# Optimization experiments

Measured on AMD Instinct MI355X. Metric: run time of the kernel, lower is better.

The kernel has to match this reference:

```python
import jax, jax.numpy as jnp
import numpy as np
import math

DIM = 1024      # dim == dim_attn (required by value-reshape)
HEAD = 16
KV = 128        # K_v routing slots
HD = DIM // HEAD
N = 50000       # number of nodes


def setup_inputs() -> dict:
    key = jax.random.key(0)
    ks = jax.random.split(key, 8)
    s = lambda fan_in: 1.0 / np.sqrt(fan_in)
    return {
        "x": jax.random.normal(ks[0], (N, DIM), jnp.float32),
        "node_index": jax.random.normal(ks[1], (N, 4), jnp.float32),
        # nn.Linear(dim, dim_attn)
        "Wq": jax.random.normal(ks[2], (DIM, DIM), jnp.float32) * s(DIM),
        "bq": jnp.zeros((DIM,), jnp.float32),
        # nn.Parameter key (K_v, head, head_dim), torch.randn init
        "key_p": jax.random.normal(ks[3], (KV, HEAD, HD), jnp.float32),
        # nn.Linear(dim, dim)
        "Wv": jax.random.normal(ks[4], (DIM, DIM), jnp.float32) * s(DIM),
        "bv": jnp.zeros((DIM,), jnp.float32),
        # gate params, shape (head, 1)
        "alpha": jnp.full((HEAD, 1), math.log(9.0), jnp.float32),
        "beta": jnp.full((HEAD, 1), math.log(0.01), jnp.float32),
        # nn.Linear(4, head*K_v)
        "Wb": jax.random.normal(ks[5], (HEAD * KV, 4), jnp.float32) * s(4),
        "bb": jnp.zeros((HEAD * KV,), jnp.float32),
    }


def _mh_sinkhorn(A, num_iters=3, eps=0.05):
    # A: (N, H, K). Faithful to the per-head torch sinkhorn (Q transposed to
    # (K, N)): row sums are over the node axis, col sums over the slot axis.
    n = A.shape[0]
    k = A.shape[2]
    Q = jnp.exp(A / eps)
    Q = Q / jnp.sum(Q, axis=(0, 2), keepdims=True)          # total-sum norm per head
    for _ in range(num_iters):
        Q = Q / jnp.sum(Q, axis=0, keepdims=True) / k       # rows of Q.T (per slot)
        Q = Q / jnp.sum(Q, axis=2, keepdims=True) / n       # cols of Q.T (per node)
    return Q * n


def reference(x, node_index, Wq, bq, key_p, Wv, bv, alpha, beta, Wb, bb):
    n = x.shape[0]
    q = (x @ Wq.T + bq).reshape(n, HEAD, HD)
    attn = jnp.einsum('nhd,rhd->nhr', q, key_p) / np.float32(np.sqrt(HD))
    bias = (node_index @ Wb.T + bb).reshape(n, HEAD, KV)
    attn = attn + bias                                       # (n, H, K_v)
    xv = (x @ Wv.T + bv).reshape(n, HEAD, HD)
    v = jnp.einsum('nhr,nhd->rhd', jax.nn.sigmoid(attn), xv)  # (K_v, H, D)
    cons = _mh_sinkhorn(jax.nn.softmax(attn, axis=-1))
    v = jnp.einsum('nhr,rhd->nhd', cons, v)
    out = jax.nn.sigmoid(alpha) * xv + jax.nn.sigmoid(beta) * v  # (H,1) broadcasts
    return out.reshape(n, DIM)
```

## Files before the change

### kernel.cpp

```cpp
#include <hip/hip_runtime.h>

#define N_NODES 50000
#define MPAD    50176
#define DIM     1024
#define HEAD    16
#define KV      128
#define HD      64
#define NGRP    98

typedef unsigned short ushort_t;
typedef short short8 __attribute__((ext_vector_type(8)));
typedef float f32x4 __attribute__((ext_vector_type(4)));

__device__ inline unsigned short f2bf(float f){
  union { float f; unsigned u; } v; v.f = f;
  unsigned u = v.u;
  unsigned r = (u + 0x7FFFu + ((u >> 16) & 1u)) >> 16;
  return (unsigned short)r;
}
__device__ inline float bf2f(unsigned u16){
  union { unsigned u; float f; } v; v.u = (u16 & 0xFFFFu) << 16; return v.f;
}

__device__ inline void gload_lds16(const void* g, void* l){
  __builtin_amdgcn_global_load_lds(
      (const __attribute__((address_space(1))) void*)g,
      (__attribute__((address_space(3))) void*)l, 16, 0, 0);
}

__device__ inline short8 frag64(const ushort_t* lds, int row, int kk, int lane){
  int c  = kk*4 + (lane >> 4);
  int cc = c ^ (row & 7);
  return *(const short8*)(lds + row*64 + cc*8);
}
__device__ inline short8 frag128(const ushort_t* lds, int row, int kk, int lane){
  int c  = kk*4 + (lane >> 4);
  int cc = c ^ (row & 7);
  return *(const short8*)(lds + row*128 + cc*8);
}

__global__ void k_zero(float* p, int n){
  int i = blockIdx.x*256 + threadIdx.x;
  if (i < n) p[i] = 0.f;
}

__global__ void k_prep_x(const float* __restrict__ x, ushort_t* __restrict__ x_bf){
  int idx = blockIdx.x*256 + threadIdx.x;
  int row = idx >> 7, c = idx & 127;
  const float4* s = (const float4*)(x + (size_t)row*1024 + c*8);
  float4 f0 = s[0], f1 = s[1];
  short8 v;
  v[0]=(short)f2bf(f0.x); v[1]=(short)f2bf(f0.y); v[2]=(short)f2bf(f0.z); v[3]=(short)f2bf(f0.w);
  v[4]=(short)f2bf(f1.x); v[5]=(short)f2bf(f1.y); v[6]=(short)f2bf(f1.z); v[7]=(short)f2bf(f1.w);
  int sc = (c & ~7) | ((c ^ row) & 7);
  *(short8*)(x_bf + (size_t)row*1024 + sc*8) = v;
}

__global__ void k_prep_w(const float* __restrict__ Wq, const float* __restrict__ Wv,
                         ushort_t* __restrict__ w_bf){
  int idx = blockIdx.x*256 + threadIdx.x;
  int j = idx >> 10, k = idx & 1023;
  float v = (j < 1024) ? Wq[idx] : Wv[(size_t)(j-1024)*1024 + k];
  int d = k & 63;
  int scol = (k & ~63) | ((((d>>3) ^ (j & 7)) & 7) << 3) | (d & 7);
  w_bf[(size_t)j*1024 + scol] = f2bf(v);
}

__global__ void k_prep_key(const float* __restrict__ key_p, ushort_t* __restrict__ key_bf){
  int idx = blockIdx.x*256 + threadIdx.x;
  int h = idx >> 13, rem = idx & 8191;
  int r = rem >> 6, d = rem & 63;
  float v = key_p[(size_t)(r*HEAD + h)*HD + d];
  int pos = ((((d>>3) ^ (r & 7)) & 7) << 3) | (d & 7);
  key_bf[(size_t)h*8192 + r*64 + pos] = f2bf(v);
}

__global__ void k_vreduce(const float* __restrict__ vp, float* __restrict__ vout){
  int i = blockIdx.x*256 + threadIdx.x;
  float s = 0.f;
  for (int gg = 0; gg < NGRP; ++gg) s += vp[(size_t)gg*131072 + i];
  vout[i] = s;
}

template<int HALF>
__global__ __launch_bounds__(512) void k_gemm(const ushort_t* __restrict__ x_bf,
    const ushort_t* __restrict__ w_bf, const float* __restrict__ bq,
    const float* __restrict__ bv, ushort_t* __restrict__ q_bf, float* xv_out){
  extern __shared__ char gsm[];
  ushort_t* As = (ushort_t*)gsm;
  ushort_t* Bs = (ushort_t*)(gsm + 65536);
  const int tid = threadIdx.x, lane = tid & 63;
  const int wid = tid >> 6, wr = wid >> 2, wc = wid & 3;
  int b = blockIdx.x;
  int wg = (b & 7)*98 + (b >> 3);
  const int bm0 = (wg >> 2) * 256;
  const int bn0 = HALF*1024 + (wg & 3) * 256;

  f32x4 acc[8][4];
  #pragma unroll
  for (int m=0;m<8;m++)
    #pragma unroll
    for (int n=0;n<4;n++) acc[m][n] = (f32x4){0.f,0.f,0.f,0.f};

  const ushort_t* asrc = x_bf + (size_t)bm0*1024;
  const ushort_t* bsrc = w_bf + (size_t)bn0*1024;

#define STAGE(kt, bi)                                                    \
  { _Pragma("unroll")                                                    \
    for (int it=0; it<4; ++it){                                          \
      int chunk = it*512 + tid;                                          \
      int r = chunk >> 3, c = chunk & 7;                                 \
      gload_lds16(asrc + (size_t)r*1024 + (kt)*64 + c*8,                 \
                  As + (bi)*16384 + chunk*8);                            \
    }                                                                    \
    _Pragma("unroll")                                                    \
    for (int it=0; it<4; ++it){                                          \
      int chunk = it*512 + tid;                                          \
      int r = chunk >> 3, c = chunk & 7;                                 \
      gload_lds16(bsrc + (size_t)r*1024 + (kt)*64 + c*8,                 \
                  Bs + (bi)*16384 + chunk*8);                            \
    }                                                                    \
  }

  STAGE(0, 0);
  STAGE(1, 1);

  for (int kt = 0; kt < 16; ++kt){
    const int cur = kt & 1;
    if (kt == 15) { asm volatile("s_waitcnt vmcnt(0)" ::: "memory"); }
    else          { asm volatile("s_waitcnt vmcnt(8)" ::: "memory"); }
    __builtin_amdgcn_s_barrier();

    const ushort_t* ab  = As + cur*16384;
    const ushort_t* bb_ = Bs + cur*16384;
    #pragma unroll
    for (int kk=0;kk<2;kk++){
      short8 bfr[4];
      #pragma unroll
      for (int n=0;n<4;n++) bfr[n] = frag64(bb_, wc*64 + n*16 + (lane&15), kk, lane);
      #pragma unroll
      for (int m=0;m<8;m++){
        short8 af = frag64(ab, wr*128 + m*16 + (lane&15), kk, lane);
        #pragma unroll
        for (int n=0;n<4;n++)
          acc[m][n] = __builtin_amdgcn_mfma_f32_16x16x32_bf16(af, bfr[n], acc[m][n], 0,0,0);
      }
    }
    __builtin_amdgcn_s_barrier();
    if (kt + 2 < 16) STAGE(kt+2, cur);
  }
#undef STAGE

  __syncthreads();

  float biasv[4];
  #pragma unroll
  for (int n=0;n<4;n++){
    int col = bn0 + wc*64 + n*16 + (lane & 15);
    biasv[n] = (HALF == 0) ? bq[col] : bv[col - 1024];
  }

  if (HALF == 0){
    ushort_t* img = (ushort_t*)gsm;
    #pragma unroll
    for (int n=0;n<4;n++){
      int lcol = wc*64 + n*16 + (lane & 15);
      int d = lcol & 63;
      #pragma unroll
      for (int m=0;m<8;m++){
        #pragma unroll
        for (int j=0;j<4;j++){
          int lrow = wr*128 + m*16 + (lane>>4)*4 + j;
          int sc = (lcol & ~63) | ((((d>>3) ^ (lrow & 7)) & 7) << 3) | (d & 7);
          img[lrow*256 + sc] = f2bf(acc[m][n][j] + biasv[n]);
        }
      }
    }
    __syncthreads();
    #pragma unroll
    for (int it=0; it<16; ++it){
      int r  = it*16 + (tid >> 5);
      int ch = tid & 31;
      short8 v = *(const short8*)(img + r*256 + ch*8);
      *(short8*)(q_bf + (size_t)(bm0 + r)*1024 + bn0 + ch*8) = v;
    }
  } else {
    #pragma unroll
    for (int n=0;n<4;n++){
      int col = bn0 + wc*64 + n*16 + (lane & 15);
      #pragma unroll
      for (int m=0;m<8;m++){
        #pragma unroll
        for (int j=0;j<4;j++){
          int row = bm0 + wr*128 + m*16 + (lane>>4)*4 + j;
          if (row < N_NODES)
            xv_out[(size_t)row*1024 + (col - 1024)] = acc[m][n][j] + biasv[n];
        }
      }
    }
  }
}

__global__ __launch_bounds__(256) void k_s1(const ushort_t* __restrict__ q_bf,
    const ushort_t* __restrict__ key_bf, const float* __restrict__ ni,
    const float* __restrict__ Wb, const float* __restrict__ bb,
    const float* __restrict__ cs_in, float* __restrict__ cs_out){
  __shared__ ushort_t key_lds[128*64];
  __shared__ float col_acc[4][128];
  const int tid = threadIdx.x, lane = tid & 63, wid = tid >> 6;
  const int h   = blockIdx.x & 15;
  const int blk = blockIdx.x >> 4;
  const int gw  = blk*4 + wid;
  const int cl  = lane & 15, rg = lane >> 4;

  #pragma unroll
  for (int it = 0; it < 4; ++it){
    int chunk = it*256 + tid;
    gload_lds16(key_bf + (size_t)h*8192 + chunk*8, key_lds + chunk*8);
  }

  float wbv[8][4], bbr[8], wv[8];
  #pragma unroll
  for (int n=0;n<8;n++){
    int r = h*128 + n*16 + cl;
    float4 w4 = *(const float4*)(Wb + (size_t)r*4);
    wbv[n][0]=w4.x; wbv[n][1]=w4.y; wbv[n][2]=w4.z; wbv[n][3]=w4.w;
    bbr[n] = bb[r];
    wv[n]  = 1.f/(128.f*cs_in[r]);
  }
  float cs_acc[8];
  #pragma unroll
  for (int n=0;n<8;n++) cs_acc[n] = 0.f;

  __syncthreads();

  const int g0 = gw*4;
  short8 qc[2], qn[2];
  { int row = g0*16 + cl;
    #pragma unroll
    for (int kk=0;kk<2;kk++){
      int c = (kk*4+rg) ^ (row & 7);
      qc[kk] = *(const short8*)(q_bf + (size_t)row*1024 + h*64 + c*8);
    } }

  for (int u = 0; u < 4; ++u){
    const int i0 = (g0+u)*16;
    if (u+1 < 4){
      int row = i0 + 16 + cl;
      #pragma unroll
      for (int kk=0;kk<2;kk++){
        int c = (kk*4+rg) ^ (row & 7);
        qn[kk] = *(const short8*)(q_bf + (size_t)row*1024 + h*64 + c*8);
      }
    }
    float4 ni4[4];
    #pragma unroll
    for (int j=0;j<4;j++){
      int row = i0 + rg*4 + j;
      if (row < N_NODES) ni4[j] = *(const float4*)(ni + (size_t)row*4);
      else { ni4[j].x=0.f; ni4[j].y=0.f; ni4[j].z=0.f; ni4[j].w=0.f; }
    }
    f32x4 acc[8];
    #pragma unroll
    for (int n=0;n<8;n++) acc[n] = (f32x4){0.f,0.f,0.f,0.f};
    #pragma unroll
    for (int n=0;n<8;n++){
      short8 k0 = frag64(key_lds, n*16+cl, 0, lane);
      short8 k1 = frag64(key_lds, n*16+cl, 1, lane);
      acc[n] = __builtin_amdgcn_mfma_f32_16x16x32_bf16(qc[0], k0, acc[n], 0,0,0);
      acc[n] = __builtin_amdgcn_mfma_f32_16x16x32_bf16(qc[1], k1, acc[n], 0,0,0);
    }
    float a[8][4];
    #pragma unroll
    for (int n=0;n<8;n++)
      #pragma unroll
      for (int j=0;j<4;j++)
        a[n][j] = acc[n][j]*0.125f
                + wbv[n][0]*ni4[j].x + wbv[n][1]*ni4[j].y
                + wbv[n][2]*ni4[j].z + wbv[n][3]*ni4[j].w + bbr[n];

    float mj[4], sj[4];
    #pragma unroll
    for (int j=0;j<4;j++){
      float m0 = a[0][j];
      #pragma unroll
      for (int n=1;n<8;n++) m0 = fmaxf(m0, a[n][j]);
      m0 = fmaxf(m0, __shfl_xor(m0,1));
      m0 = fmaxf(m0, __shfl_xor(m0,2));
      m0 = fmaxf(m0, __shfl_xor(m0,4));
      m0 = fmaxf(m0, __shfl_xor(m0,8));
      mj[j] = m0;
    }
    #pragma unroll
    for (int j=0;j<4;j++){
      float s = 0.f;
      #pragma unroll
      for (int n=0;n<8;n++){ float e = __expf(a[n][j]-mj[j]); a[n][j]=e; s+=e; }
      s += __shfl_xor(s,1); s += __shfl_xor(s,2);
      s += __shfl_xor(s,4); s += __shfl_xor(s,8);
      sj[j] = s;
    }
    #pragma unroll
    for (int j=0;j<4;j++){
      float inv = 20.f/sj[j];
      #pragma unroll
      for (int n=0;n<8;n++) a[n][j] = __expf(a[n][j]*inv);
    }
    float uj[4];
    #pragma unroll
    for (int j=0;j<4;j++){
      float s = 0.f;
      #pragma unroll
      for (int n=0;n<8;n++) s += a[n][j]*wv[n];
      s += __shfl_xor(s,1); s += __shfl_xor(s,2);
      s += __shfl_xor(s,4); s += __shfl_xor(s,8);
      int row = i0 + rg*4 + j;
      uj[j] = (row < N_NODES) ? 1.f/(50000.f*s) : 0.f;
    }
    #pragma unroll
    for (int n=0;n<8;n++)
      cs_acc[n] += a[n][0]*uj[0] + a[n][1]*uj[1] + a[n][2]*uj[2] + a[n][3]*uj[3];

    qc[0] = qn[0]; qc[1] = qn[1];
  }

  #pragma unroll
  for (int n=0;n<8;n++){
    float v = cs_acc[n];
    v += __shfl_xor(v,16); v += __shfl_xor(v,32);
    cs_acc[n] = v;
  }
  if (rg == 0){
    #pragma unroll
    for (int n=0;n<8;n++) col_acc[wid][n*16+cl] = cs_acc[n];
  }
  __syncthreads();
  if (tid < 128)
    atomicAdd(&cs_out[h*128+tid],
      col_acc[0][tid]+col_acc[1][tid]+col_acc[2][tid]+col_acc[3][tid]);
}

__global__ __launch_bounds__(256) void k_s2(const ushort_t* __restrict__ q_bf,
    const ushort_t* __restrict__ key_bf, const float* __restrict__ ni,
    const float* __restrict__ Wb, const float* __restrict__ bb,
    const float* __restrict__ cs_in, const float* __restrict__ v_fin,
    float* xv_out, const float* __restrict__ alpha, const float* __restrict__ beta){
  __shared__ ushort_t key_lds[128*64];
  __shared__ ushort_t vT[64*128];
  __shared__ ushort_t consW[4][16*128];
  const int tid = threadIdx.x, lane = tid & 63, wid = tid >> 6;
  const int h   = blockIdx.x & 15;
  const int blk = blockIdx.x >> 4;
  const int gw  = blk*4 + wid;
  const int cl  = lane & 15, rg = lane >> 4;

  #pragma unroll
  for (int it = 0; it < 4; ++it){
    int chunk = it*256 + tid;
    gload_lds16(key_bf + (size_t)h*8192 + chunk*8, key_lds + chunk*8);
  }
  { int r = tid >> 1, dh = (tid & 1)*32;
    #pragma unroll
    for (int i=0;i<32;i++){
      int d = dh + i;
      vT[d*128 + ((r>>3) ^ (d&7))*8 + (r&7)] = f2bf(v_fin[((size_t)r*16 + h)*64 + d]);
    } }

  float wbv[8][4], bbr[8], wv[8];
  #pragma unroll
  for (int n=0;n<8;n++){
    int r = h*128 + n*16 + cl;
    float4 w4 = *(const float4*)(Wb + (size_t)r*4);
    wbv[n][0]=w4.x; wbv[n][1]=w4.y; wbv[n][2]=w4.z; wbv[n][3]=w4.w;
    bbr[n] = bb[r];
    wv[n]  = 1.f/(128.f*cs_in[r]);
  }
  const float sa = 1.f/(1.f + __expf(-alpha[h]));
  const float sb = 1.f/(1.f + __expf(-beta[h]));

  __syncthreads();

  ushort_t* cw = consW[wid];
  const int g0 = gw*4;
  short8 qc[2], qn[2];
  { int row = g0*16 + cl;
    #pragma unroll
    for (int kk=0;kk<2;kk++){
      int c = (kk*4+rg) ^ (row & 7);
      qc[kk] = *(const short8*)(q_bf + (size_t)row*1024 + h*64 + c*8);
    } }

  for (int u = 0; u < 4; ++u){
    const int i0 = (g0+u)*16;
    if (u+1 < 4){
      int row = i0 + 16 + cl;
      #pragma unroll
      for (int kk=0;kk<2;kk++){
        int c = (kk*4+rg) ^ (row & 7);
        qn[kk] = *(const short8*)(q_bf + (size_t)row*1024 + h*64 + c*8);
      }
    }
    float4 ni4[4];
    #pragma unroll
    for (int j=0;j<4;j++){
      int row = i0 + rg*4 + j;
      if (row < N_NODES) ni4[j] = *(const float4*)(ni + (size_t)row*4);
      else { ni4[j].x=0.f; ni4[j].y=0.f; ni4[j].z=0.f; ni4[j].w=0.f; }
    }
    f32x4 acc[8];
    #pragma unroll
    for (int n=0;n<8;n++) acc[n] = (f32x4){0.f,0.f,0.f,0.f};
    #pragma unroll
    for (int n=0;n<8;n++){
      short8 k0 = frag64(key_lds, n*16+cl, 0, lane);
      short8 k1 = frag64(key_lds, n*16+cl, 1, lane);
      acc[n] = __builtin_amdgcn_mfma_f32_16x16x32_bf16(qc[0], k0, acc[n], 0,0,0);
      acc[n] = __builtin_amdgcn_mfma_f32_16x16x32_bf16(qc[1], k1, acc[n], 0,0,0);
    }
    float a[8][4];
    #pragma unroll
    for (int n=0;n<8;n++)
      #pragma unroll
      for (int j=0;j<4;j++)
        a[n][j] = acc[n][j]*0.125f
                + wbv[n][0]*ni4[j].x + wbv[n][1]*ni4[j].y
                + wbv[n][2]*ni4[j].z + wbv[n][3]*ni4[j].w + bbr[n];

    float mj[4], sj[4];
    #pragma unroll
    for (int j=0;j<4;j++){
      float m0 = a[0][j];
      #pragma unroll
      for (int n=1;n<8;n++) m0 = fmaxf(m0, a[n][j]);
      m0 = fmaxf(m0, __shfl_xor(m0,1));
      m0 = fmaxf(m0, __shfl_xor(m0,2));
      m0 = fmaxf(m0, __shfl_xor(m0,4));
      m0 = fmaxf(m0, __shfl_xor(m0,8));
      mj[j] = m0;
    }
    #pragma unroll
    for (int j=0;j<4;j++){
      float s = 0.f;
      #pragma unroll
      for (int n=0;n<8;n++){ float e = __expf(a[n][j]-mj[j]); a[n][j]=e; s+=e; }
      s += __shfl_xor(s,1); s += __shfl_xor(s,2);
      s += __shfl_xor(s,4); s += __shfl_xor(s,8);
      sj[j] = s;
    }
    #pragma unroll
    for (int j=0;j<4;j++){
      float inv = 20.f/sj[j];
      #pragma unroll
      for (int n=0;n<8;n++) a[n][j] = __expf(a[n][j]*inv);
    }
    float scj[4];
    #pragma unroll
    for (int j=0;j<4;j++){
      float s = 0.f;
      #pragma unroll
      for (int n=0;n<8;n++) s += a[n][j]*wv[n];
      s += __shfl_xor(s,1); s += __shfl_xor(s,2);
      s += __shfl_xor(s,4); s += __shfl_xor(s,8);
      scj[j] = 1.f/s;
    }
    #pragma unroll
    for (int n=0;n<8;n++){
      #pragma unroll
      for (int j=0;j<4;j++){
        int node = rg*4 + j;
        int r = n*16 + cl;
        int ch = (r>>3) ^ (node & 7);
        cw[node*128 + ch*8 + (r&7)] = f2bf(scj[j]*a[n][j]*wv[n]);
      }
    }
    f32x4 oac[4];
    #pragma unroll
    for (int nf=0;nf<4;nf++) oac[nf] = (f32x4){0.f,0.f,0.f,0.f};
    #pragma unroll
    for (int ks=0; ks<4; ++ks){
      short8 ca = frag128(cw, cl, ks, lane);
      #pragma unroll
      for (int nf=0;nf<4;nf++){
        short8 vb = frag128(vT, nf*16+cl, ks, lane);
        oac[nf] = __builtin_amdgcn_mfma_f32_16x16x32_bf16(ca, vb, oac[nf], 0,0,0);
      }
    }
    #pragma unroll
    for (int j=0;j<4;j++){
      int row = i0 + rg*4 + j;
      if (row < N_NODES){
        #pragma unroll
        for (int nf=0;nf<4;nf++){
          size_t ad = (size_t)row*1024 + h*64 + nf*16 + cl;
          xv_out[ad] = sa*xv_out[ad] + sb*oac[nf][j];
        }
      }
    }
    qc[0] = qn[0]; qc[1] = qn[1];
  }
}

template<int PHASE>
__global__ __launch_bounds__(256) void k_attn(
    const ushort_t* __restrict__ q_bf, const ushort_t* __restrict__ key_bf,
    const float* __restrict__ node_index, const float* __restrict__ Wb,
    const float* __restrict__ bb, const float* __restrict__ colsum_in,
    float* __restrict__ colsum_out, const float* __restrict__ v_fin,
    float* __restrict__ v_part, float* xv_out,
    const float* __restrict__ alpha, const float* __restrict__ beta)
{
  constexpr int QB    = 2;
  constexpr int O_Q   = 0;
  constexpr int O_KEY = O_Q + QB*8192;
  constexpr int O_NI  = O_KEY + 16384;
  constexpr int O_WB  = O_NI + QB*1024;
  constexpr int O_RED = O_WB + 2560;
  constexpr int O_COL = O_RED + 2048;
  constexpr int O_W   = O_COL + 512;
  constexpr int O_X1  = O_W + 512;
  constexpr int O_X2  = O_X1 + 16384;

  extern __shared__ char smem[];
  ushort_t* q_lds   = (ushort_t*)(smem + O_Q);
  ushort_t* key_lds = (ushort_t*)(smem + O_KEY);
  float* ni_lds  = (float*)(smem + O_NI);
  float* wb_lds  = (float*)(smem + O_WB);
  float* red_lds = (float*)(smem + O_RED);
  float* col_acc = (float*)(smem + O_COL);
  ushort_t* sigT = (ushort_t*)(smem + O_X1);
  ushort_t* xvT  = (ushort_t*)(smem + O_X2);

  const int tid = threadIdx.x, lane = tid & 63, wid = tid >> 6;
  const int h    = blockIdx.x & 15;
  const int g    = blockIdx.x >> 4;
  const int base = g * 512;
  int NT = (MPAD - base) >> 6; if (NT > 8) NT = 8;

  #pragma unroll
  for (int it = 0; it < 4; ++it){
    int chunk = it*256 + tid;
    gload_lds16(key_bf + (size_t)h*8192 + chunk*8, key_lds + chunk*8);
  }
  #pragma unroll
  for (int it = 0; it < 2; ++it){
    int chunk = it*256 + tid;
    int r = chunk >> 3, c = chunk & 7;
    gload_lds16(q_bf + (size_t)(base + r)*1024 + h*64 + c*8, q_lds + chunk*8);
  }
  { int r = tid >> 2, c = tid & 3;
    ni_lds[tid] = (base + r < N_NODES) ? node_index[(size_t)(base + r)*4 + c] : 0.f; }
  if (tid < 128){
    #pragma unroll
    for (int c=0;c<4;c++) wb_lds[tid*5+c] = Wb[(size_t)(h*128 + tid)*4 + c];
    wb_lds[tid*5+4] = bb[h*128 + tid];
    col_acc[tid] = 0.f;
  }
  float xvr[16], xvn[16];
  { int d = tid & 63, q4 = tid >> 6;
    #pragma unroll
    for (int i=0;i<16;i++){
      int row = base + q4*16 + i;
      xvr[i] = (row < N_NODES) ? xv_out[(size_t)row*1024 + h*64 + d] : 0.f;
    } }
  f32x4 vac[2][4];
  for (int m=0;m<2;m++) for (int n=0;n<4;n++) vac[m][n] = (f32x4){0.f,0.f,0.f,0.f};

  __syncthreads();

  for (int t = 0; t < NT; ++t){
    const int i0  = base + t*64;
    const int cur = t & 1;
    const ushort_t* qb  = q_lds  + cur*4096;
    const float*    nib = ni_lds + cur*256;
    float ni_next = 0.f;

    if (t+1 < NT){
      int i1 = i0 + 64;
      #pragma unroll
      for (int it = 0; it < 2; ++it){
        int chunk = it*256 + tid;
        int r = chunk >> 3, c = chunk & 7;
        gload_lds16(q_bf + (size_t)(i1 + r)*1024 + h*64 + c*8,
                    q_lds + (cur^1)*4096 + chunk*8);
      }
      int r = tid >> 2, c = tid & 3;
      ni_next = (i0 + 64 + r < N_NODES) ? node_index[(size_t)(i0+64+r)*4 + c] : 0.f;
      int d = tid & 63, q4 = tid >> 6;
      #pragma unroll
      for (int i=0;i<16;i++){
        int row = i0 + 64 + q4*16 + i;
        xvn[i] = (row < N_NODES) ? xv_out[(size_t)row*1024 + h*64 + d] : 0.f;
      }
    }

    f32x4 acc[2][4];
    for (int m=0;m<2;m++) for (int n=0;n<4;n++) acc[m][n] = (f32x4){0.f,0.f,0.f,0.f};
    #pragma unroll
    for (int kk = 0; kk < 2; ++kk){
      short8 kf[2];
      #pragma unroll
      for (int m=0;m<2;m++) kf[m] = frag64(key_lds, wid*32 + m*16 + (lane&15), kk, lane);
      #pragma unroll
      for (int n=0;n<4;n++){
        short8 qf = frag64(qb, n*16 + (lane&15), kk, lane);
        #pragma unroll
        for (int m=0;m<2;m++)
          acc[m][n] = __builtin_amdgcn_mfma_f32_16x16x32_bf16(kf[m], qf, acc[m][n], 0,0,0);
      }
    }

    float nif[4][4];
    #pragma unroll
    for (int n=0;n<4;n++){
      int nn = n*16 + (lane&15);
      #pragma unroll
      for (int c=0;c<4;c++) nif[n][c] = nib[nn*4+c];
    }
    float a[2][4][4];
    #pragma unroll
    for (int m=0;m<2;m++){
      #pragma unroll
      for (int j=0;j<4;j++){
        int r = wid*32 + m*16 + (lane>>4)*4 + j;
        float w0 = wb_lds[r*5+0], w1 = wb_lds[r*5+1];
        float w2 = wb_lds[r*5+2], w3 = wb_lds[r*5+3], w4 = wb_lds[r*5+4];
        #pragma unroll
        for (int n=0;n<4;n++){
          float b = w4 + w0*nif[n][0] + w1*nif[n][1] + w2*nif[n][2] + w3*nif[n][3];
          a[m][n][j] = acc[m][n][j]*0.125f + b;
        }
      }
    }

    float vmask[4];
    #pragma unroll
    for (int n=0;n<4;n++) vmask[n] = (i0 + n*16 + (lane&15) < N_NODES) ? 1.f : 0.f;

    #pragma unroll
    for (int m=0;m<2;m++) for (int n=0;n<4;n++) for (int j=0;j<4;j++){
      int r  = wid*32 + m*16 + (lane>>4)*4 + j;
      int nn = n*16 + (lane&15);
      float sg = vmask[n] / (1.f + __expf(-a[m][n][j]));
      sigT[r*64 + ((((nn>>3) ^ (r&7)) & 7) << 3) + (nn&7)] = f2bf(sg);
    }
    { int d = tid & 63, q4 = tid >> 6;
      #pragma unroll
      for (int i=0;i<16;i++){
        int nn = q4*16 + i;
        xvT[d*64 + ((((nn>>3) ^ (d&7)) & 7) << 3) + (nn&7)] = f2bf(xvr[i]);
      }
    }

    float pm[4];
    #pragma unroll
    for (int n=0;n<4;n++){
      float m0 = a[0][n][0];
      #pragma unroll
      for (int m=0;m<2;m++) for (int j=0;j<4;j++) m0 = fmaxf(m0, a[m][n][j]);
      m0 = fmaxf(m0, __shfl_xor(m0, 16));
      m0 = fmaxf(m0, __shfl_xor(m0, 32));
      pm[n] = m0;
    }
    if (lane < 16){
      #pragma unroll
      for (int n=0;n<4;n++) red_lds[wid*64 + n*16 + lane] = pm[n];
    }
    __syncthreads();

    float mnn[4], snn[4];
    #pragma unroll
    for (int n=0;n<4;n++){
      int nn = n*16 + (lane&15);
      float m0 = red_lds[nn];
      m0 = fmaxf(m0, red_lds[64+nn]); m0 = fmaxf(m0, red_lds[128+nn]); m0 = fmaxf(m0, red_lds[192+nn]);
      mnn[n] = m0;
    }
    #pragma unroll
    for (int n=0;n<4;n++){
      float s = 0.f;
      #pragma unroll
      for (int m=0;m<2;m++) for (int j=0;j<4;j++){
        float e = __expf(a[m][n][j] - mnn[n]);
        a[m][n][j] = e; s += e;
      }
      s += __shfl_xor(s, 16); s += __shfl_xor(s, 32);
      snn[n] = s;
    }
    if (lane < 16){
      #pragma unroll
      for (int n=0;n<4;n++) red_lds[256 + wid*64 + n*16 + lane] = snn[n];
    }

    #pragma unroll
    for (int kk=0;kk<2;kk++){
      short8 sa[2];
      #pragma unroll
      for (int m=0;m<2;m++) sa[m] = frag64(sigT, wid*32 + m*16 + (lane&15), kk, lane);
      #pragma unroll
      for (int n=0;n<4;n++){
        short8 xf = frag64(xvT, n*16 + (lane&15), kk, lane);
        #pragma unroll
        for (int m=0;m<2;m++)
          vac[m][n] = __builtin_amdgcn_mfma_f32_16x16x32_bf16(sa[m], xf, vac[m][n], 0,0,0);
      }
    }
    __syncthreads();

    #pragma unroll
    for (int n=0;n<4;n++){
      int nn = n*16 + (lane&15);
      snn[n] = red_lds[256+nn] + red_lds[256+64+nn] + red_lds[256+128+nn] + red_lds[256+192+nn];
    }
    #pragma unroll
    for (int n=0;n<4;n++){
      float inv = 20.f / snn[n];
      #pragma unroll
      for (int m=0;m<2;m++) for (int j=0;j<4;j++)
        a[m][n][j] = __expf(a[m][n][j] * inv);
    }

    float cs[2][4];
    #pragma unroll
    for (int m=0;m<2;m++){
      #pragma unroll
      for (int j=0;j<4;j++){
        float s = 0.f;
        #pragma unroll
        for (int n=0;n<4;n++) s += a[m][n][j] * vmask[n];
        s += __shfl_xor(s, 1); s += __shfl_xor(s, 2);
        s += __shfl_xor(s, 4); s += __shfl_xor(s, 8);
        cs[m][j] = s;
      }
    }
    if ((lane & 15) == 0){
      #pragma unroll
      for (int m=0;m<2;m++) for (int j=0;j<4;j++){
        int r = wid*32 + m*16 + (lane>>4)*4 + j;
        col_acc[r] += cs[m][j];
      }
    }

    if (t+1 < NT){
      ni_lds[(cur^1)*256 + tid] = ni_next;
      #pragma unroll
      for (int i=0;i<16;i++) xvr[i] = xvn[i];
    }
    __syncthreads();
  }

  { float* vdst = v_part + (size_t)g*131072;
    #pragma unroll
    for (int m=0;m<2;m++) for (int n=0;n<4;n++) for (int j=0;j<4;j++){
      int r = wid*32 + m*16 + (lane>>4)*4 + j;
      int d = n*16 + (lane&15);
      vdst[((size_t)r*16 + h)*64 + d] = vac[m][n][j];
    } }
  if (tid < 128) atomicAdd(&colsum_out[h*128 + tid], col_acc[tid]);
}

extern "C" void kernel_launch(void* const* d_in, const int* in_sizes, int n_in,
                              void* d_out, int out_size, void* d_ws, size_t ws_size,
                              hipStream_t stream){
  const float* x     = (const float*)d_in[0];
  const float* ni    = (const float*)d_in[1];
  const float* Wq    = (const float*)d_in[2];
  const float* bq    = (const float*)d_in[3];
  const float* keyp  = (const float*)d_in[4];
  const float* Wv    = (const float*)d_in[5];
  const float* bv    = (const float*)d_in[6];
  const float* alpha = (const float*)d_in[7];
  const float* beta  = (const float*)d_in[8];
  const float* Wb    = (const float*)d_in[9];
  const float* bb    = (const float*)d_in[10];
  float* out = (float*)d_out;

  char* ws = (char*)d_ws;
  ushort_t* x_bf   = (ushort_t*)(ws);
  float*    v_part = (float*)(ws);
  ushort_t* q_bf   = (ushort_t*)(ws + 102760448);
  ushort_t* w_bf   = (ushort_t*)(ws + 205520896);
  ushort_t* key_bf = (ushort_t*)(ws + 209715200);
  float*    v_fin  = (float*)(ws + 209977344);
  float*    cs     = (float*)(ws + 210501632);

  (void)hipFuncSetAttribute((const void*)k_gemm<0>,
      hipFuncAttributeMaxDynamicSharedMemorySize, 131072);
  (void)hipFuncSetAttribute((const void*)k_gemm<1>,
      hipFuncAttributeMaxDynamicSharedMemorySize, 131072);

  k_zero<<<dim3(24), 256, 0, stream>>>(cs, 6144);
  k_zero<<<dim3(704), 256, 0, stream>>>((float*)(x_bf + (size_t)N_NODES*1024), 90112);
  k_prep_x<<<dim3(25000), 256, 0, stream>>>(x, x_bf);
  k_prep_w<<<dim3(2048*1024/256), 256, 0, stream>>>(Wq, Wv, w_bf);
  k_prep_key<<<dim3(HEAD*KV*HD/256), 256, 0, stream>>>(keyp, key_bf);
  k_gemm<0><<<dim3(784), 512, 131072, stream>>>(x_bf, w_bf, bq, bv, q_bf, out);
  k_gemm<1><<<dim3(784), 512, 131072, stream>>>(x_bf, w_bf, bq, bv, q_bf, out);

  dim3 ag(NGRP*16);
  k_attn<0><<<ag, 256, 65024, stream>>>(q_bf, key_bf, ni, Wb, bb, nullptr, cs, v_fin, v_part, out, alpha, beta);
  k_vreduce<<<dim3(512), 256, 0, stream>>>(v_part, v_fin);
  k_s1<<<dim3(3136), 256, 0, stream>>>(q_bf, key_bf, ni, Wb, bb, cs,      cs+2048);
  k_s1<<<dim3(3136), 256, 0, stream>>>(q_bf, key_bf, ni, Wb, bb, cs+2048, cs+4096);
  k_s2<<<dim3(3136), 256, 0, stream>>>(q_bf, key_bf, ni, Wb, bb, cs+4096, v_fin, out, alpha, beta);
}
```

Before: 935.4 us.

## Fold positional bias into MFMA via augmented bf16 split operands, transpose score tile

The node_index @ Wb bias is computed with an extra MFMA per slot block. Augmented node features and bias weights (ones column, bf16 hi/lo residual split, pre-scaled by 8) are built in two new prep kernels. The score tile is transposed (key as A operand) so each lane holds one node and all slots it needs. Softmax reductions then become mostly in-register with two cross-lane shuffles, the max-subtraction is dropped, and k_s2 writes packed weights. In exchange it adds prep launches and extra memory traffic for ni_aug, and dropping the max subtraction risks overflow if logits grow large.

```diff
diff --git a/kernel.cpp b/kernel.cpp
--- a/kernel.cpp
+++ b/kernel.cpp
@@ -73,6 +73,33 @@
   float v = key_p[(size_t)(r*HEAD + h)*HD + d];
   int pos = ((((d>>3) ^ (r & 7)) & 7) << 3) | (d & 7);
   key_bf[(size_t)h*8192 + r*64 + pos] = f2bf(v);
+}
+
+__global__ void k_prep_wbk(const float* __restrict__ Wb, const float* __restrict__ bb,
+                           ushort_t* __restrict__ wbk){
+  int idx = blockIdx.x*256 + threadIdx.x;
+  int hr = idx >> 5, c = idx & 31;
+  float v = 0.f;
+  if (c < 4)        v = 8.f*Wb[(size_t)hr*4 + c];
+  else if (c == 4)  v = 8.f*bb[hr];
+  else if (c < 9)   v = 8.f*Wb[(size_t)hr*4 + (c-5)];
+  else if (c < 13){ float w = 8.f*Wb[(size_t)hr*4 + (c-9)]; v = w - bf2f(f2bf(w)); }
+  else if (c == 13){ float w = 8.f*bb[hr]; v = w - bf2f(f2bf(w)); }
+  wbk[idx] = f2bf(v);
+}
+
+__global__ void k_prep_ni(const float* __restrict__ ni, ushort_t* __restrict__ ni_aug){
+  int idx = blockIdx.x*256 + threadIdx.x;
+  int row = idx >> 5, c = idx & 31;
+  float v = 0.f;
+  if (row < N_NODES){
+    if (c < 4)        v = ni[(size_t)row*4 + c];
+    else if (c == 4)  v = 1.f;
+    else if (c < 9){  float x0 = ni[(size_t)row*4 + (c-5)]; v = x0 - bf2f(f2bf(x0)); }
+    else if (c < 13)  v = ni[(size_t)row*4 + (c-9)];
+    else if (c == 13) v = 1.f;
+  }
+  ni_aug[idx] = f2bf(v);
 }
 
 __global__ void k_vreduce(const float* __restrict__ vp, float* __restrict__ vout){
@@ -202,8 +229,8 @@
 }
 
 __global__ __launch_bounds__(256) void k_s1(const ushort_t* __restrict__ q_bf,
-    const ushort_t* __restrict__ key_bf, const float* __restrict__ ni,
-    const float* __restrict__ Wb, const float* __restrict__ bb,
+    const ushort_t* __restrict__ key_bf, const ushort_t* __restrict__ wbk,
+    const ushort_t* __restrict__ ni_aug,
     const float* __restrict__ cs_in, float* __restrict__ cs_out){
   __shared__ ushort_t key_lds[128*64];
   __shared__ float col_acc[4][128];
@@ -218,19 +245,20 @@
     int chunk = it*256 + tid;
     gload_lds16(key_bf + (size_t)h*8192 + chunk*8, key_lds + chunk*8);
   }
-
-  float wbv[8][4], bbr[8], wv[8];
-  #pragma unroll
-  for (int n=0;n<8;n++){
-    int r = h*128 + n*16 + cl;
-    float4 w4 = *(const float4*)(Wb + (size_t)r*4);
-    wbv[n][0]=w4.x; wbv[n][1]=w4.y; wbv[n][2]=w4.z; wbv[n][3]=w4.w;
-    bbr[n] = bb[r];
-    wv[n]  = 1.f/(128.f*cs_in[r]);
-  }
-  float cs_acc[8];
-  #pragma unroll
-  for (int n=0;n<8;n++) cs_acc[n] = 0.f;
+  short8 kfb[8];
+  #pragma unroll
+  for (int rb=0;rb<8;rb++)
+    kfb[rb] = *(const short8*)(wbk + (size_t)h*4096 + (rb*16+cl)*32 + rg*8);
+  float wv[8][4];
+  #pragma unroll
+  for (int rb=0;rb<8;rb++){
+    float4 c4 = *(const float4*)(cs_in + h*128 + rb*16 + rg*4);
+    wv[rb][0]=1.f/(128.f*c4.x); wv[rb][1]=1.f/(128.f*c4.y);
+    wv[rb][2]=1.f/(128.f*c4.z); wv[rb][3]=1.f/(128.f*c4.w);
+  }
+  float csa[8][4];
+  #pragma unroll
+  for (int rb=0;rb<8;rb++) for (int j=0;j<4;j++) csa[rb][j] = 0.f;
 
   __syncthreads();
 
@@ -253,86 +281,61 @@
         qn[kk] = *(const short8*)(q_bf + (size_t)row*1024 + h*64 + c*8);
       }
     }
-    float4 ni4[4];
+    short8 nif = *(const short8*)(ni_aug + (size_t)(i0+cl)*32 + rg*8);
+    f32x4 acc[8];
+    #pragma unroll
+    for (int rb=0;rb<8;rb++){
+      acc[rb] = __builtin_amdgcn_mfma_f32_16x16x32_bf16(kfb[rb], nif,
+                    (f32x4){0.f,0.f,0.f,0.f}, 0,0,0);
+      short8 k0 = frag64(key_lds, rb*16+cl, 0, lane);
+      short8 k1 = frag64(key_lds, rb*16+cl, 1, lane);
+      acc[rb] = __builtin_amdgcn_mfma_f32_16x16x32_bf16(k0, qc[0], acc[rb], 0,0,0);
+      acc[rb] = __builtin_amdgcn_mfma_f32_16x16x32_bf16(k1, qc[1], acc[rb], 0,0,0);
+    }
+    float a[8][4];
+    float S = 0.f;
+    #pragma unroll
+    for (int rb=0;rb<8;rb++)
+      #pragma unroll
+      for (int j=0;j<4;j++){
+        float e = __expf(acc[rb][j]*0.125f);
+        a[rb][j] = e; S += e;
+      }
+    S += __shfl_xor(S,16); S += __shfl_xor(S,32);
+    float z = 20.f/S;
+    float Sw = 0.f;
+    #pragma unroll
+    for (int rb=0;rb<8;rb++)
+      #pragma unroll
+      for (int j=0;j<4;j++){
+        float t = __expf(a[rb][j]*z);
+        a[rb][j] = t; Sw += t*wv[rb][j];
+      }
+    Sw += __shfl_xor(Sw,16); Sw += __shfl_xor(Sw,32);
+    float uu = (i0 + cl < N_NODES) ? 1.f/(50000.f*Sw) : 0.f;
+    #pragma unroll
+    for (int rb=0;rb<8;rb++)
+      #pragma unroll
+      for (int j=0;j<4;j++) csa[rb][j] += a[rb][j]*uu;
+
+    qc[0] = qn[0]; qc[1] = qn[1];
+  }
+
+  #pragma unroll
+  for (int rb=0;rb<8;rb++)
     #pragma unroll
     for (int j=0;j<4;j++){
-      int row = i0 + rg*4 + j;
-      if (row < N_NODES) ni4[j] = *(const float4*)(ni + (size_t)row*4);
-      else { ni4[j].x=0.f; ni4[j].y=0.f; ni4[j].z=0.f; ni4[j].w=0.f; }
-    }
-    f32x4 acc[8];
-    #pragma unroll
-    for (int n=0;n<8;n++) acc[n] = (f32x4){0.f,0.f,0.f,0.f};
-    #pragma unroll
-    for (int n=0;n<8;n++){
-      short8 k0 = frag64(key_lds, n*16+cl, 0, lane);
-      short8 k1 = frag64(key_lds, n*16+cl, 1, lane);
-      acc[n] = __builtin_amdgcn_mfma_f32_16x16x32_bf16(qc[0], k0, acc[n], 0,0,0);
-      acc[n] = __builtin_amdgcn_mfma_f32_16x16x32_bf16(qc[1], k1, acc[n], 0,0,0);
-    }
-    float a[8][4];
-    #pragma unroll
-    for (int n=0;n<8;n++)
+      float v = csa[rb][j];
+      v += __shfl_xor(v,1); v += __shfl_xor(v,2);
+      v += __shfl_xor(v,4); v += __shfl_xor(v,8);
+      csa[rb][j] = v;
+    }
+  if (cl == 0){
+    #pragma unroll
+    for (int rb=0;rb<8;rb++)
       #pragma unroll
       for (int j=0;j<4;j++)
-        a[n][j] = acc[n][j]*0.125f
-                + wbv[n][0]*ni4[j].x + wbv[n][1]*ni4[j].y
-                + wbv[n][2]*ni4[j].z + wbv[n][3]*ni4[j].w + bbr[n];
-
-    float mj[4], sj[4];
-    #pragma unroll
-    for (int j=0;j<4;j++){
-      float m0 = a[0][j];
-      #pragma unroll
-      for (int n=1;n<8;n++) m0 = fmaxf(m0, a[n][j]);
-      m0 = fmaxf(m0, __shfl_xor(m0,1));
-      m0 = fmaxf(m0, __shfl_xor(m0,2));
-      m0 = fmaxf(m0, __shfl_xor(m0,4));
-      m0 = fmaxf(m0, __shfl_xor(m0,8));
-      mj[j] = m0;
-    }
-    #pragma unroll
-    for (int j=0;j<4;j++){
-      float s = 0.f;
-      #pragma unroll
-      for (int n=0;n<8;n++){ float e = __expf(a[n][j]-mj[j]); a[n][j]=e; s+=e; }
-      s += __shfl_xor(s,1); s += __shfl_xor(s,2);
-      s += __shfl_xor(s,4); s += __shfl_xor(s,8);
-      sj[j] = s;
-    }
-    #pragma unroll
-    for (int j=0;j<4;j++){
-      float inv = 20.f/sj[j];
-      #pragma unroll
-      for (int n=0;n<8;n++) a[n][j] = __expf(a[n][j]*inv);
-    }
-    float uj[4];
-    #pragma unroll
-    for (int j=0;j<4;j++){
-      float s = 0.f;
-      #pragma unroll
-      for (int n=0;n<8;n++) s += a[n][j]*wv[n];
-      s += __shfl_xor(s,1); s += __shfl_xor(s,2);
-      s += __shfl_xor(s,4); s += __shfl_xor(s,8);
-      int row = i0 + rg*4 + j;
-      uj[j] = (row < N_NODES) ? 1.f/(50000.f*s) : 0.f;
-    }
-    #pragma unroll
-    for (int n=0;n<8;n++)
-      cs_acc[n] += a[n][0]*uj[0] + a[n][1]*uj[1] + a[n][2]*uj[2] + a[n][3]*uj[3];
-
-    qc[0] = qn[0]; qc[1] = qn[1];
-  }
-
-  #pragma unroll
-  for (int n=0;n<8;n++){
-    float v = cs_acc[n];
-    v += __shfl_xor(v,16); v += __shfl_xor(v,32);
-    cs_acc[n] = v;
-  }
-  if (rg == 0){
-    #pragma unroll
-    for (int n=0;n<8;n++) col_acc[wid][n*16+cl] = cs_acc[n];
+        col_acc[wid][rb*16 + rg*4 + j] = csa[rb][j];
   }
   __syncthreads();
   if (tid < 128)
@@ -341,8 +344,8 @@
 }
 
 __global__ __launch_bounds__(256) void k_s2(const ushort_t* __restrict__ q_bf,
-    const ushort_t* __restrict__ key_bf, const float* __restrict__ ni,
-    const float* __restrict__ Wb, const float* __restrict__ bb,
+    const ushort_t* __restrict__ key_bf, const ushort_t* __restrict__ wbk,
+    const ushort_t* __restrict__ ni_aug,
     const float* __restrict__ cs_in, const float* __restrict__ v_fin,
     float* xv_out, const float* __restrict__ alpha, const float* __restrict__ beta){
   __shared__ ushort_t key_lds[128*64];
@@ -365,15 +368,16 @@
       int d = dh + i;
       vT[d*128 + ((r>>3) ^ (d&7))*8 + (r&7)] = f2bf(v_fin[((size_t)r*16 + h)*64 + d]);
     } }
-
-  float wbv[8][4], bbr[8], wv[8];
-  #pragma unroll
-  for (int n=0;n<8;n++){
-    int r = h*128 + n*16 + cl;
-    float4 w4 = *(const float4*)(Wb + (size_t)r*4);
-    wbv[n][0]=w4.x; wbv[n][1]=w4.y; wbv[n][2]=w4.z; wbv[n][3]=w4.w;
-    bbr[n] = bb[r];
-    wv[n]  = 1.f/(128.f*cs_in[r]);
+  short8 kfb[8];
+  #pragma unroll
+  for (int rb=0;rb<8;rb++)
+    kfb[rb] = *(const short8*)(wbk + (size_t)h*4096 + (rb*16+cl)*32 + rg*8);
+  float wv[8][4];
+  #pragma unroll
+  for (int rb=0;rb<8;rb++){
+    float4 c4 = *(const float4*)(cs_in + h*128 + rb*16 + rg*4);
+    wv[rb][0]=1.f/(128.f*c4.x); wv[rb][1]=1.f/(128.f*c4.y);
+    wv[rb][2]=1.f/(128.f*c4.z); wv[rb][3]=1.f/(128.f*c4.w);
   }
   const float sa = 1.f/(1.f + __expf(-alpha[h]));
   const float sb = 1.f/(1.f + __expf(-beta[h]));
@@ -400,78 +404,49 @@
         qn[kk] = *(const short8*)(q_bf + (size_t)row*1024 + h*64 + c*8);
       }
     }
-    float4 ni4[4];
-    #pragma unroll
-    for (int j=0;j<4;j++){
-      int row = i0 + rg*4 + j;
-      if (row < N_NODES) ni4[j] = *(const float4*)(ni + (size_t)row*4);
-      else { ni4[j].x=0.f; ni4[j].y=0.f; ni4[j].z=0.f; ni4[j].w=0.f; }
-    }
+    short8 nif = *(const short8*)(ni_aug + (size_t)(i0+cl)*32 + rg*8);
     f32x4 acc[8];
     #pragma unroll
-    for (int n=0;n<8;n++) acc[n] = (f32x4){0.f,0.f,0.f,0.f};
-    #pragma unroll
-    for (int n=0;n<8;n++){
-      short8 k0 = frag64(key_lds, n*16+cl, 0, lane);
-      short8 k1 = frag64(key_lds, n*16+cl, 1, lane);
-      acc[n] = __builtin_amdgcn_mfma_f32_16x16x32_bf16(qc[0], k0, acc[n], 0,0,0);
-      acc[n] = __builtin_amdgcn_mfma_f32_16x16x32_bf16(qc[1], k1, acc[n], 0,0,0);
+    for (int rb=0;rb<8;rb++){
+      acc[rb] = __builtin_amdgcn_mfma_f32_16x16x32_bf16(kfb[rb], nif,
+                    (f32x4){0.f,0.f,0.f,0.f}, 0,0,0);
+      short8 k0 = frag64(key_lds, rb*16+cl, 0, lane);
+      short8 k1 = frag64(key_lds, rb*16+cl, 1, lane);
+      acc[rb] = __builtin_amdgcn_mfma_f32_16x16x32_bf16(k0, qc[0], acc[rb], 0,0,0);
+      acc[rb] = __builtin_amdgcn_mfma_f32_16x16x32_bf16(k1, qc[1], acc[rb], 0,0,0);
     }
     float a[8][4];
-    #pragma unroll
-    for (int n=0;n<8;n++)
-      #pragma unroll
-      for (int j=0;j<4;j++)
-        a[n][j] = acc[n][j]*0.125f
-                + wbv[n][0]*ni4[j].x + wbv[n][1]*ni4[j].y
-                + wbv[n][2]*ni4[j].z + wbv[n][3]*ni4[j].w + bbr[n];
-
-    float mj[4], sj[4];
-    #pragma unroll
-    for (int j=0;j<4;j++){
-      float m0 = a[0][j];
-      #pragma unroll
-      for (int n=1;n<8;n++) m0 = fmaxf(m0, a[n][j]);
-      m0 = fmaxf(m0, __shfl_xor(m0,1));
-      m0 = fmaxf(m0, __shfl_xor(m0,2));
-      m0 = fmaxf(m0, __shfl_xor(m0,4));
-      m0 = fmaxf(m0, __shfl_xor(m0,8));
-      mj[j] = m0;
-    }
-    #pragma unroll
-    for (int j=0;j<4;j++){
-      float s = 0.f;
-      #pragma unroll
-      for (int n=0;n<8;n++){ float e = __expf(a[n][j]-mj[j]); a[n][j]=e; s+=e; }
-      s += __shfl_xor(s,1); s += __shfl_xor(s,2);
-      s += __shfl_xor(s,4); s += __shfl_xor(s,8);
-      sj[j] = s;
-    }
-    #pragma unroll
-    for (int j=0;j<4;j++){
-      float inv = 20.f/sj[j];
-      #pragma unroll
-      for (int n=0;n<8;n++) a[n][j] = __expf(a[n][j]*inv);
-    }
-    float scj[4];
-    #pragma unroll
-    for (int j=0;j<4;j++){
-      float s = 0.f;
-      #pragma unroll
-      for (int n=0;n<8;n++) s += a[n][j]*wv[n];
-      s += __shfl_xor(s,1); s += __shfl_xor(s,2);
-      s += __shfl_xor(s,4); s += __shfl_xor(s,8);
-      scj[j] = 1.f/s;
-    }
-    #pragma unroll
-    for (int n=0;n<8;n++){
+    float S = 0.f;
+    #pragma unroll
+    for (int rb=0;rb<8;rb++)
       #pragma unroll
       for (int j=0;j<4;j++){
-        int node = rg*4 + j;
-        int r = n*16 + cl;
-        int ch = (r>>3) ^ (node & 7);
-        cw[node*128 + ch*8 + (r&7)] = f2bf(scj[j]*a[n][j]*wv[n]);
-      }
+        float e = __expf(acc[rb][j]*0.125f);
+        a[rb][j] = e; S += e;
+      }
+    S += __shfl_xor(S,16); S += __shfl_xor(S,32);
+    float z = 20.f/S;
+    float Sw = 0.f;
+    #pragma unroll
+    for (int rb=0;rb<8;rb++)
+      #pragma unroll
+      for (int j=0;j<4;j++){
+        float t = __expf(a[rb][j]*z);
+        a[rb][j] = t; Sw += t*wv[rb][j];
+      }
+    Sw += __shfl_xor(Sw,16); Sw += __shfl_xor(Sw,32);
+    float scale = 1.f/Sw;
+
+    #pragma unroll
+    for (int rb=0;rb<8;rb++){
+      int r0 = rb*16 + rg*4;
+      unsigned lo = (unsigned)f2bf(scale*a[rb][0]*wv[rb][0])
+                  | ((unsigned)f2bf(scale*a[rb][1]*wv[rb][1]) << 16);
+      unsigned hi = (unsigned)f2bf(scale*a[rb][2]*wv[rb][2])
+                  | ((unsigned)f2bf(scale*a[rb][3]*wv[rb][3]) << 16);
+      uint2 pv; pv.x = lo; pv.y = hi;
+      int ch = (r0 >> 3) ^ (cl & 7);
+      *(uint2*)(cw + cl*128 + ch*8 + (r0 & 7)) = pv;
     }
     f32x4 oac[4];
     #pragma unroll
@@ -782,6 +757,8 @@
   ushort_t* key_bf = (ushort_t*)(ws + 209715200);
   float*    v_fin  = (float*)(ws + 209977344);
   float*    cs     = (float*)(ws + 210501632);
+  ushort_t* ni_aug = (ushort_t*)(ws + 210526208);
+  ushort_t* wbk    = (ushort_t*)(ws + 213737472);
 
   (void)hipFuncSetAttribute((const void*)k_gemm<0>,
       hipFuncAttributeMaxDynamicSharedMemorySize, 131072);
@@ -793,13 +770,15 @@
   k_prep_x<<<dim3(25000), 256, 0, stream>>>(x, x_bf);
   k_prep_w<<<dim3(2048*1024/256), 256, 0, stream>>>(Wq, Wv, w_bf);
   k_prep_key<<<dim3(HEAD*KV*HD/256), 256, 0, stream>>>(keyp, key_bf);
+  k_prep_wbk<<<dim3(256), 256, 0, stream>>>(Wb, bb, wbk);
+  k_prep_ni<<<dim3(MPAD*32/256), 256, 0, stream>>>(ni, ni_aug);
   k_gemm<0><<<dim3(784), 512, 131072, stream>>>(x_bf, w_bf, bq, bv, q_bf, out);
   k_gemm<1><<<dim3(784), 512, 131072, stream>>>(x_bf, w_bf, bq, bv, q_bf, out);
 
   dim3 ag(NGRP*16);
   k_attn<0><<<ag, 256, 65024, stream>>>(q_bf, key_bf, ni, Wb, bb, nullptr, cs, v_fin, v_part, out, alpha, beta);
   k_vreduce<<<dim3(512), 256, 0, stream>>>(v_part, v_fin);
-  k_s1<<<dim3(3136), 256, 0, stream>>>(q_bf, key_bf, ni, Wb, bb, cs,      cs+2048);
-  k_s1<<<dim3(3136), 256, 0, stream>>>(q_bf, key_bf, ni, Wb, bb, cs+2048, cs+4096);
-  k_s2<<<dim3(3136), 256, 0, stream>>>(q_bf, key_bf, ni, Wb, bb, cs+4096, v_fin, out, alpha, beta);
-}
+  k_s1<<<dim3(3136), 256, 0, stream>>>(q_bf, key_bf, wbk, ni_aug, cs,      cs+2048);
+  k_s1<<<dim3(3136), 256, 0, stream>>>(q_bf, key_bf, wbk, ni_aug, cs+2048, cs+4096);
+  k_s2<<<dim3(3136), 256, 0, stream>>>(q_bf, key_bf, wbk, ni_aug, cs+4096, v_fin, out, alpha, beta);
+}
```

Result: slower. 1.141 ms (+22.0%).
